# Kernel tuning notes

Hardware: AMD Instinct MI355X
Metric: run time of the kernel (lower is better)

## Reference

```python
import jax, jax.numpy as jnp
import numpy as np

R, N, B = 3, 8192, 4096
IN_DIM, HID, OUT = 256, 128, 64
EPS = 1e-5


def _bn(x, g, b):
    # BatchNorm1d in training mode: biased batch stats over dim 0
    m = jnp.mean(x, axis=0)
    v = jnp.var(x, axis=0)
    return (x - m) * jax.lax.rsqrt(v + EPS) * g + b


def setup_inputs() -> dict:
    key = jax.random.key(0)
    k1, k2, k3, k4, k5 = jax.random.split(key, 5)
    features = jax.random.normal(k1, (N, IN_DIM), dtype=jnp.float32)
    u = jax.random.uniform(k2, (R, N, N), dtype=jnp.float32)
    adj = (u < 0.01).astype(jnp.float32)
    batch_nodes = jax.random.randint(k3, (B,), 0, N, dtype=jnp.int32)
    w1 = jax.random.uniform(k4, (IN_DIM, HID), dtype=jnp.float32)  # torch.rand init
    w2 = jax.random.uniform(k5, (HID, OUT), dtype=jnp.float32)
    return {
        "features": features, "adj": adj, "batch_nodes": batch_nodes,
        "w1": w1, "w2": w2,
        "gamma1": jnp.ones((IN_DIM,), jnp.float32), "beta1": jnp.zeros((IN_DIM,), jnp.float32),
        "gamma2": jnp.ones((OUT,), jnp.float32), "beta2": jnp.zeros((OUT,), jnp.float32),
    }


def reference(features, adj, batch_nodes, w1, w2, gamma1, beta1, gamma2, beta2):
    # gather batch subgraph
    x = features[batch_nodes]                       # [B, IN_DIM]
    bA = jnp.take(jnp.take(adj, batch_nodes, axis=1), batch_nodes, axis=2)  # [R, B, B]
    xn = _bn(x, gamma1, beta1)                      # shared across relations

    def per_relation(badj):
        A = badj + jnp.eye(B, dtype=badj.dtype)
        # D_mx.inverse().sqrt() of a diagonal degree matrix == diag(deg^-1/2)
        dinv = jax.lax.rsqrt(jnp.sum(A, axis=1))    # [B]
        A_hat = A * dinv[:, None] * dinv[None, :]   # D^-1/2 A D^-1/2
        h1 = jax.nn.sigmoid(jax.nn.elu((A_hat @ xn) @ w1))   # conv1 + sigmoid
        h2 = jax.nn.elu((A_hat @ h1) @ w2)                   # conv2
        return _bn(h2, gamma2, beta2)

    embed = jax.vmap(per_relation)(bA)              # [R, B, OUT]
    return jax.nn.relu(jnp.mean(embed, axis=0))     # [B, OUT]
```

## Files before the change

kernel.cpp:

```cpp
#include <hip/hip_runtime.h>
#include <hip/hip_bf16.h>

#define RR 3
#define NN 8192
#define BB 4096
#define IN_DIM 256
#define HID 128
#define OUT 64
#define CAPD 128
#define EPS 1e-5f
#define MWN (NN / 64)
#define MLPB 16

__global__ __launch_bounds__(256) void k1_bn1_prep_k(const float* __restrict__ feat,
                                                     const int* __restrict__ bn,
                                                     const float* __restrict__ g1,
                                                     const float* __restrict__ b1,
                                                     float* __restrict__ af,
                                                     float* __restrict__ bfv,
                                                     unsigned long long* __restrict__ memb,
                                                     unsigned short* __restrict__ rankg,
                                                     unsigned short* __restrict__ nodeof,
                                                     float* __restrict__ multf,
                                                     int* __restrict__ Ucnt,
                                                     unsigned short* __restrict__ pos2slot) {
    __shared__ int smult[NN];
    __shared__ unsigned short srank[NN];
    __shared__ unsigned long long smemb[MWN];
    __shared__ int sbase[MWN + 1];
    __shared__ float ps[4], pq[4];
    int t = threadIdx.x;
    if (blockIdx.x < IN_DIM) {
        int c = blockIdx.x;
        float s = 0.f, q = 0.f;
        for (int i = t; i < BB; i += 256) {
            float v = feat[(size_t)bn[i] * IN_DIM + c];
            s += v; q += v * v;
        }
        int lane = t & 63, wv = t >> 6;
        for (int o = 32; o; o >>= 1) { s += __shfl_down(s, o); q += __shfl_down(q, o); }
        if (lane == 0) { ps[wv] = s; pq[wv] = q; }
        __syncthreads();
        if (t == 0) {
            float S = ps[0] + ps[1] + ps[2] + ps[3];
            float Q = pq[0] + pq[1] + pq[2] + pq[3];
            float m = S / BB;
            float rs = rsqrtf(Q / BB - m * m + EPS);
            float a = rs * g1[c];
            af[c]  = a;
            bfv[c] = b1[c] - m * a;
        }
        return;
    }
    for (int u = t; u < NN; u += 256) smult[u] = 0;
    __syncthreads();
    for (int i = t; i < BB; i += 256) atomicAdd(&smult[bn[i]], 1);
    __syncthreads();
    if (t < MWN) {
        unsigned long long w = 0;
        for (int b = 0; b < 64; ++b) if (smult[t * 64 + b]) w |= (1ull << b);
        smemb[t] = w;
        memb[t] = w;
    }
    __syncthreads();
    if (t == 0) {
        int acc = 0;
        for (int m = 0; m < MWN; ++m) { sbase[m] = acc; acc += (int)__popcll(smemb[m]); }
        sbase[MWN] = acc;
        *Ucnt = acc;
    }
    __syncthreads();
    if (t < MWN) {
        unsigned long long w = smemb[t];
        int p = sbase[t];
        while (w) {
            int b = __builtin_ctzll(w); w &= w - 1;
            int u = t * 64 + b;
            srank[u] = (unsigned short)p;
            rankg[u] = (unsigned short)p;
            nodeof[p] = (unsigned short)u;
            multf[p]  = (float)smult[u];
            ++p;
        }
    }
    __syncthreads();
    for (int i = t; i < BB; i += 256) pos2slot[i] = srank[bn[i]];
}

__global__ __launch_bounds__(256) void build_k(const float* __restrict__ adj,
                                               const unsigned short* __restrict__ nodeof,
                                               const int* __restrict__ Ucnt,
                                               const unsigned long long* __restrict__ memb,
                                               const unsigned short* __restrict__ rankg,
                                               const float* __restrict__ multf,
                                               unsigned* __restrict__ cols,
                                               int* __restrict__ cnt,
                                               float* __restrict__ dinv) {
    int blk = blockIdx.x;
    int r = blk >> 12, s = blk & (BB - 1);
    if (s >= *Ucnt) return;
    int u = nodeof[s];
    __shared__ unsigned char nib[2048];
    __shared__ unsigned int rawb[256];
    __shared__ unsigned long long sel[MWN];
    __shared__ int sbase[MWN + 1];
    __shared__ float pdeg[4];
    int t = threadIdx.x;
    const float4* ar4 = (const float4*)(adj + ((size_t)r * NN + u) * NN);
    #pragma unroll
    for (int ch = 0; ch < 8; ++ch) {
        float4 v = ar4[ch * 256 + t];
        nib[ch * 256 + t] = (unsigned char)((v.x != 0.f) | ((v.y != 0.f) << 1) |
                                            ((v.z != 0.f) << 2) | ((v.w != 0.f) << 3));
    }
    __syncthreads();
    {
        unsigned long long x = *(const unsigned long long*)&nib[t * 8];
        x = (x | (x >> 4))  & 0x00FF00FF00FF00FFull;
        x = (x | (x >> 8))  & 0x0000FFFF0000FFFFull;
        x = (x | (x >> 16));
        rawb[t] = (unsigned int)x;
    }
    __syncthreads();
    if (t < MWN) {
        unsigned long long w = ((unsigned long long)rawb[2 * t + 1] << 32) | rawb[2 * t];
        sel[t] = w & memb[t];
    }
    __syncthreads();
    if (t < 64) {
        int p0 = (int)__popcll(sel[2 * t]);
        int p1 = (int)__popcll(sel[2 * t + 1]);
        int x = p0 + p1, xs = x;
        for (int o = 1; o < 64; o <<= 1) { int y = __shfl_up(xs, o); if (t >= o) xs += y; }
        sbase[2 * t]     = xs - x;
        sbase[2 * t + 1] = xs - p1;
        if (t == 63) sbase[MWN] = xs;
    }
    __syncthreads();
    float wdeg = 0.f;
    if (t < MWN) {
        unsigned long long w = sel[t];
        int p = sbase[t];
        unsigned* cb = cols + (size_t)blk * CAPD;
        while (w) {
            int b = __builtin_ctzll(w); w &= w - 1;
            int v = t * 64 + b;
            int rv = rankg[v];
            if (p < CAPD) cb[p] = ((unsigned)rv << 13) | (unsigned)v;
            wdeg += multf[rv];
            ++p;
        }
    }
    int lane = t & 63, wv = t >> 6;
    for (int o = 32; o; o >>= 1) wdeg += __shfl_down(wdeg, o);
    if (lane == 0) pdeg[wv] = wdeg;
    __syncthreads();
    if (t == 0) {
        int tot = sbase[MWN];
        cnt[blk] = tot < CAPD ? tot : CAPD;
        dinv[blk] = rsqrtf(pdeg[0] + pdeg[1] + pdeg[2] + pdeg[3] + 1.0f);
    }
}

__global__ __launch_bounds__(256) void agg1_k(const float* __restrict__ feat,
                                              const unsigned* __restrict__ cols,
                                              const int* __restrict__ cnt,
                                              const float* __restrict__ dinv,
                                              const float* __restrict__ multf,
                                              const unsigned short* __restrict__ nodeof,
                                              const int* __restrict__ Ucnt,
                                              const float* __restrict__ af,
                                              const float* __restrict__ bfv,
                                              float* __restrict__ y1) {
    int blk = blockIdx.x;
    int r = blk >> 12, s = blk & (BB - 1);
    if (s >= *Ucnt) return;
    int c = threadIdx.x;
    __shared__ unsigned short snode[CAPD];
    __shared__ float swl[CAPD];
    int n = cnt[blk];
    if (c < n) {
        unsigned e = cols[(size_t)blk * CAPD + c];
        int sl = e >> 13;
        snode[c] = (unsigned short)(e & 8191u);
        swl[c] = multf[sl] * dinv[(r << 12) + sl];
    }
    __syncthreads();
    float di = dinv[blk];
    float acc = di * feat[(size_t)nodeof[s] * IN_DIM + c];
    float sw = 0.f;
    #pragma unroll 4
    for (int k = 0; k < n; ++k) {
        float w = swl[k];
        sw += w;
        acc += w * feat[(size_t)snode[k] * IN_DIM + c];
    }
    float raw = acc * di;
    float f = di * (di + sw);
    y1[(size_t)blk * IN_DIM + c] = af[c] * raw + bfv[c] * f;
}

__global__ __launch_bounds__(256) void mlp1_k(const float* __restrict__ y1,
                                              const int* __restrict__ Ucnt,
                                              const float* __restrict__ w1,
                                              float* __restrict__ h1) {
    int blk = blockIdx.x;
    int r = blk / (BB / MLPB), base = (blk % (BB / MLPB)) * MLPB;
    int U = *Ucnt;
    if (base >= U) return;
    int t = threadIdx.x;
    __shared__ float ys[MLPB][IN_DIM];
    #pragma unroll
    for (int s = 0; s < MLPB; ++s) {
        int slot = base + s;
        ys[s][t] = (slot < U) ? y1[((size_t)(r << 12) + slot) * IN_DIM + t] : 0.f;
    }
    __syncthreads();
    int c = t & 127, g = t >> 7;
    float acc[8] = {0.f};
    for (int k = 0; k < IN_DIM; ++k) {
        float wv = w1[k * HID + c];
        #pragma unroll
        for (int j = 0; j < 8; ++j) acc[j] += ys[g * 8 + j][k] * wv;
    }
    #pragma unroll
    for (int j = 0; j < 8; ++j) {
        int slot = base + g * 8 + j;
        if (slot < U) {
            float z = acc[j];
            float e = z > 0.f ? z : expm1f(z);
            h1[((size_t)(r << 12) + slot) * HID + c] = 1.f / (1.f + expf(-e));
        }
    }
}

__global__ __launch_bounds__(128) void agg2_k(const float* __restrict__ h1,
                                              const unsigned* __restrict__ cols,
                                              const int* __restrict__ cnt,
                                              const float* __restrict__ dinv,
                                              const float* __restrict__ multf,
                                              const int* __restrict__ Ucnt,
                                              float* __restrict__ y2) {
    int blk = blockIdx.x;
    int r = blk >> 12, s = blk & (BB - 1);
    if (s >= *Ucnt) return;
    int c = threadIdx.x;
    __shared__ unsigned short scl[CAPD];
    __shared__ float swl[CAPD];
    int n = cnt[blk];
    if (c < n) {
        unsigned e = cols[(size_t)blk * CAPD + c];
        int sl = e >> 13;
        scl[c] = (unsigned short)sl;
        swl[c] = multf[sl] * dinv[(r << 12) + sl];
    }
    __syncthreads();
    const float* h1r = h1 + ((size_t)(r << 12)) * HID;
    float di = dinv[blk];
    float acc = di * h1r[(size_t)s * HID + c];
    #pragma unroll 4
    for (int k = 0; k < n; ++k) {
        acc += swl[k] * h1r[(size_t)scl[k] * HID + c];
    }
    y2[(size_t)blk * HID + c] = acc * di;
}

__global__ __launch_bounds__(256) void mlp2_k(const float* __restrict__ y2,
                                              const int* __restrict__ Ucnt,
                                              const float* __restrict__ w2,
                                              float* __restrict__ h2) {
    int blk = blockIdx.x;
    int r = blk / (BB / MLPB), base = (blk % (BB / MLPB)) * MLPB;
    int U = *Ucnt;
    if (base >= U) return;
    int t = threadIdx.x;
    __shared__ float ys[MLPB][HID];
    #pragma unroll
    for (int s = t >> 7; s < MLPB; s += 2) {
        int slot = base + s;
        ys[s][t & 127] = (slot < U) ? y2[((size_t)(r << 12) + slot) * HID + (t & 127)] : 0.f;
    }
    __syncthreads();
    int c = t & 63, g = t >> 6;
    float acc[4] = {0.f};
    for (int k = 0; k < HID; ++k) {
        float wv = w2[k * OUT + c];
        #pragma unroll
        for (int j = 0; j < 4; ++j) acc[j] += ys[g * 4 + j][k] * wv;
    }
    #pragma unroll
    for (int j = 0; j < 4; ++j) {
        int slot = base + g * 4 + j;
        if (slot < U) {
            float z = acc[j];
            h2[((size_t)(r << 12) + slot) * OUT + c] = z > 0.f ? z : expm1f(z);
        }
    }
}

__global__ __launch_bounds__(256) void bn2_stats_k(const float* __restrict__ h2,
                                                   const float* __restrict__ multf,
                                                   const int* __restrict__ Ucnt,
                                                   float* __restrict__ m2,
                                                   float* __restrict__ rs2) {
    int ro = blockIdx.x;
    int r = ro >> 6, o = ro & (OUT - 1);
    int U = *Ucnt;
    float s = 0.f, q = 0.f;
    for (int sl = threadIdx.x; sl < U; sl += 256) {
        float m = multf[sl];
        float v = h2[(size_t)((r << 12) + sl) * OUT + o];
        s += m * v; q += m * v * v;
    }
    int lane = threadIdx.x & 63, wv = threadIdx.x >> 6;
    for (int off = 32; off; off >>= 1) { s += __shfl_down(s, off); q += __shfl_down(q, off); }
    __shared__ float ps[4], pq[4];
    if (lane == 0) { ps[wv] = s; pq[wv] = q; }
    __syncthreads();
    if (threadIdx.x == 0) {
        float S = ps[0] + ps[1] + ps[2] + ps[3];
        float Q = pq[0] + pq[1] + pq[2] + pq[3];
        float m = S / BB;
        float v = Q / BB - m * m;
        m2[ro] = m;
        rs2[ro] = rsqrtf(v + EPS);
    }
}

__global__ __launch_bounds__(256) void finalize_k(const float* __restrict__ h2,
                                                  const unsigned short* __restrict__ pos2slot,
                                                  const float* __restrict__ m2,
                                                  const float* __restrict__ rs2,
                                                  const float* __restrict__ g2,
                                                  const float* __restrict__ b2,
                                                  float* __restrict__ out) {
    int idx = blockIdx.x * 256 + threadIdx.x;
    if (idx >= BB * OUT) return;
    int i = idx >> 6, o = idx & (OUT - 1);
    int sl = pos2slot[i];
    float s = 0.f;
    for (int r = 0; r < RR; ++r) {
        float v = h2[(size_t)((r << 12) + sl) * OUT + o];
        s += (v - m2[r * OUT + o]) * rs2[r * OUT + o] * g2[o] + b2[o];
    }
    s *= (1.0f / RR);
    out[idx] = s > 0.f ? s : 0.f;
}

extern "C" void kernel_launch(void* const* d_in, const int* in_sizes, int n_in,
                              void* d_out, int out_size, void* d_ws, size_t ws_size,
                              hipStream_t stream) {
    const float* feat = (const float*)d_in[0];
    const float* adj  = (const float*)d_in[1];
    const int*   bn   = (const int*)d_in[2];
    const float* w1   = (const float*)d_in[3];
    const float* w2   = (const float*)d_in[4];
    const float* g1   = (const float*)d_in[5];
    const float* b1   = (const float*)d_in[6];
    const float* g2   = (const float*)d_in[7];
    const float* b2   = (const float*)d_in[8];
    float* out = (float*)d_out;

    char* ws = (char*)d_ws;
    size_t off = 0;
    auto alloc = [&](size_t bytes) { size_t o = off; off += (bytes + 255) & ~(size_t)255; return o; };
    unsigned long long* memb = (unsigned long long*)(ws + alloc(MWN * 8));
    unsigned short* rankg    = (unsigned short*)(ws + alloc(NN * 2));
    unsigned short* nodeof   = (unsigned short*)(ws + alloc(BB * 2));
    float* multf             = (float*)(ws + alloc(BB * 4));
    int* Ucnt                = (int*)(ws + alloc(4));
    unsigned short* pos2slot = (unsigned short*)(ws + alloc(BB * 2));
    float* af                = (float*)(ws + alloc(IN_DIM * 4));
    float* bfv               = (float*)(ws + alloc(IN_DIM * 4));
    float* m2                = (float*)(ws + alloc(RR * OUT * 4));
    float* rs2               = (float*)(ws + alloc(RR * OUT * 4));
    unsigned* cols           = (unsigned*)(ws + alloc((size_t)RR * BB * CAPD * 4));
    int* cnt                 = (int*)(ws + alloc((size_t)RR * BB * 4));
    float* dinv              = (float*)(ws + alloc((size_t)RR * BB * 4));
    float* y1                = (float*)(ws + alloc((size_t)RR * BB * IN_DIM * 4));
    float* h1                = (float*)(ws + alloc((size_t)RR * BB * HID * 4));
    float* y2                = (float*)(ws + alloc((size_t)RR * BB * HID * 4));
    float* h2                = (float*)(ws + alloc((size_t)RR * BB * OUT * 4));

    k1_bn1_prep_k<<<IN_DIM + 1, 256, 0, stream>>>(feat, bn, g1, b1, af, bfv,
                                                  memb, rankg, nodeof, multf, Ucnt, pos2slot);
    build_k<<<RR * BB, 256, 0, stream>>>(adj, nodeof, Ucnt, memb, rankg, multf, cols, cnt, dinv);
    agg1_k<<<RR * BB, 256, 0, stream>>>(feat, cols, cnt, dinv, multf, nodeof, Ucnt, af, bfv, y1);
    mlp1_k<<<RR * (BB / MLPB), 256, 0, stream>>>(y1, Ucnt, w1, h1);
    agg2_k<<<RR * BB, 128, 0, stream>>>(h1, cols, cnt, dinv, multf, Ucnt, y2);
    mlp2_k<<<RR * (BB / MLPB), 256, 0, stream>>>(y2, Ucnt, w2, h2);
    bn2_stats_k<<<RR * OUT, 256, 0, stream>>>(h2, multf, Ucnt, m2, rs2);
    finalize_k<<<(BB * OUT + 255) / 256, 256, 0, stream>>>(h2, pos2slot, m2, rs2, g2, b2, out);
}
```

Before: 164.9 us.

## Fuse sparse aggregation with dense MLP layers, one wave per row

Merges each aggregation kernel with the following small matmul+activation kernel, so each block of 16 rows aggregates neighbors into shared memory and then applies the weight matrix. This drops the y1/y2 intermediate buffers and two kernel launches. Each wave now handles four rows using float4 or float2 vector loads, where before each row got its own block. The trade-off is 12k blocks becoming 768 blocks, which means less parallelism for the latency-bound gathers and more shared memory per block.

```diff
diff --git a/kernel.cpp b/kernel.cpp
--- a/kernel.cpp
+++ b/kernel.cpp
@@ -10,7 +10,6 @@
 #define CAPD 128
 #define EPS 1e-5f
 #define MWN (NN / 64)
-#define MLPB 16
 
 __global__ __launch_bounds__(256) void k1_bn1_prep_k(const float* __restrict__ feat,
                                                      const int* __restrict__ bn,
@@ -162,66 +161,78 @@
     }
 }
 
-__global__ __launch_bounds__(256) void agg1_k(const float* __restrict__ feat,
-                                              const unsigned* __restrict__ cols,
-                                              const int* __restrict__ cnt,
-                                              const float* __restrict__ dinv,
-                                              const float* __restrict__ multf,
-                                              const unsigned short* __restrict__ nodeof,
-                                              const int* __restrict__ Ucnt,
-                                              const float* __restrict__ af,
-                                              const float* __restrict__ bfv,
-                                              float* __restrict__ y1) {
+__global__ __launch_bounds__(256) void aggmlp1_k(const float* __restrict__ feat,
+                                                 const unsigned* __restrict__ cols,
+                                                 const int* __restrict__ cnt,
+                                                 const float* __restrict__ dinv,
+                                                 const float* __restrict__ multf,
+                                                 const unsigned short* __restrict__ nodeof,
+                                                 const int* __restrict__ Ucnt,
+                                                 const float* __restrict__ af,
+                                                 const float* __restrict__ bfv,
+                                                 const float* __restrict__ w1,
+                                                 float* __restrict__ h1) {
     int blk = blockIdx.x;
-    int r = blk >> 12, s = blk & (BB - 1);
-    if (s >= *Ucnt) return;
-    int c = threadIdx.x;
-    __shared__ unsigned short snode[CAPD];
-    __shared__ float swl[CAPD];
-    int n = cnt[blk];
-    if (c < n) {
-        unsigned e = cols[(size_t)blk * CAPD + c];
-        int sl = e >> 13;
-        snode[c] = (unsigned short)(e & 8191u);
-        swl[c] = multf[sl] * dinv[(r << 12) + sl];
-    }
-    __syncthreads();
-    float di = dinv[blk];
-    float acc = di * feat[(size_t)nodeof[s] * IN_DIM + c];
-    float sw = 0.f;
-    #pragma unroll 4
-    for (int k = 0; k < n; ++k) {
-        float w = swl[k];
-        sw += w;
-        acc += w * feat[(size_t)snode[k] * IN_DIM + c];
-    }
-    float raw = acc * di;
-    float f = di * (di + sw);
-    y1[(size_t)blk * IN_DIM + c] = af[c] * raw + bfv[c] * f;
-}
-
-__global__ __launch_bounds__(256) void mlp1_k(const float* __restrict__ y1,
-                                              const int* __restrict__ Ucnt,
-                                              const float* __restrict__ w1,
-                                              float* __restrict__ h1) {
-    int blk = blockIdx.x;
-    int r = blk / (BB / MLPB), base = (blk % (BB / MLPB)) * MLPB;
+    int r = blk >> 8, base = (blk & 255) << 4;
     int U = *Ucnt;
     if (base >= U) return;
-    int t = threadIdx.x;
-    __shared__ float ys[MLPB][IN_DIM];
-    #pragma unroll
-    for (int s = 0; s < MLPB; ++s) {
-        int slot = base + s;
-        ys[s][t] = (slot < U) ? y1[((size_t)(r << 12) + slot) * IN_DIM + t] : 0.f;
+    int t = threadIdx.x, lane = t & 63, wv = t >> 6;
+    __shared__ unsigned short snode[16][CAPD];
+    __shared__ float swl[16][CAPD];
+    __shared__ float ys[16][IN_DIM];
+    __shared__ float sdii[16], ssw[16];
+    __shared__ int sn[16];
+    for (int s16 = wv; s16 < 16; s16 += 4) {
+        int slot = base + s16;
+        int n = (slot < U) ? cnt[(r << 12) + slot] : 0;
+        if (lane == 0) { sn[s16] = n; sdii[s16] = (slot < U) ? dinv[(r << 12) + slot] : 0.f; }
+        size_t cb = ((size_t)(r << 12) + slot) * CAPD;
+        float swsum = 0.f;
+        for (int idx = lane; idx < n; idx += 64) {
+            unsigned e = cols[cb + idx];
+            int sl = e >> 13;
+            snode[s16][idx] = (unsigned short)(e & 8191u);
+            float w = multf[sl] * dinv[(r << 12) + sl];
+            swl[s16][idx] = w;
+            swsum += w;
+        }
+        for (int o = 32; o; o >>= 1) swsum += __shfl_down(swsum, o);
+        if (lane == 0) ssw[s16] = swsum;
+    }
+    __syncthreads();
+    int c4 = lane << 2;
+    for (int j = 0; j < 4; ++j) {
+        int s16 = (wv << 2) + j;
+        int slot = base + s16;
+        if (slot >= U) { *(float4*)&ys[s16][c4] = make_float4(0.f, 0.f, 0.f, 0.f); continue; }
+        int n = sn[s16];
+        float di = sdii[s16];
+        float4 v = ((const float4*)(feat + (size_t)nodeof[slot] * IN_DIM))[lane];
+        float4 acc;
+        acc.x = di * v.x; acc.y = di * v.y; acc.z = di * v.z; acc.w = di * v.w;
+        #pragma unroll 4
+        for (int k = 0; k < n; ++k) {
+            float w = swl[s16][k];
+            float4 x = ((const float4*)(feat + (size_t)snode[s16][k] * IN_DIM))[lane];
+            acc.x += w * x.x; acc.y += w * x.y; acc.z += w * x.z; acc.w += w * x.w;
+        }
+        float f = di * (di + ssw[s16]);
+        float4 a4 = *(const float4*)(af + c4);
+        float4 b4 = *(const float4*)(bfv + c4);
+        float4 o;
+        o.x = a4.x * (acc.x * di) + b4.x * f;
+        o.y = a4.y * (acc.y * di) + b4.y * f;
+        o.z = a4.z * (acc.z * di) + b4.z * f;
+        o.w = a4.w * (acc.w * di) + b4.w * f;
+        *(float4*)&ys[s16][c4] = o;
     }
     __syncthreads();
     int c = t & 127, g = t >> 7;
     float acc[8] = {0.f};
     for (int k = 0; k < IN_DIM; ++k) {
-        float wv = w1[k * HID + c];
+        float wvl = w1[k * HID + c];
         #pragma unroll
-        for (int j = 0; j < 8; ++j) acc[j] += ys[g * 8 + j][k] * wv;
+        for (int j = 0; j < 8; ++j) acc[j] += ys[g * 8 + j][k] * wvl;
     }
     #pragma unroll
     for (int j = 0; j < 8; ++j) {
@@ -234,59 +245,63 @@
     }
 }
 
-__global__ __launch_bounds__(128) void agg2_k(const float* __restrict__ h1,
-                                              const unsigned* __restrict__ cols,
-                                              const int* __restrict__ cnt,
-                                              const float* __restrict__ dinv,
-                                              const float* __restrict__ multf,
-                                              const int* __restrict__ Ucnt,
-                                              float* __restrict__ y2) {
+__global__ __launch_bounds__(256) void aggmlp2_k(const float* __restrict__ h1,
+                                                 const unsigned* __restrict__ cols,
+                                                 const int* __restrict__ cnt,
+                                                 const float* __restrict__ dinv,
+                                                 const float* __restrict__ multf,
+                                                 const int* __restrict__ Ucnt,
+                                                 const float* __restrict__ w2,
+                                                 float* __restrict__ h2) {
     int blk = blockIdx.x;
-    int r = blk >> 12, s = blk & (BB - 1);
-    if (s >= *Ucnt) return;
-    int c = threadIdx.x;
-    __shared__ unsigned short scl[CAPD];
-    __shared__ float swl[CAPD];
-    int n = cnt[blk];
-    if (c < n) {
-        unsigned e = cols[(size_t)blk * CAPD + c];
-        int sl = e >> 13;
-        scl[c] = (unsigned short)sl;
-        swl[c] = multf[sl] * dinv[(r << 12) + sl];
-    }
-    __syncthreads();
-    const float* h1r = h1 + ((size_t)(r << 12)) * HID;
-    float di = dinv[blk];
-    float acc = di * h1r[(size_t)s * HID + c];
-    #pragma unroll 4
-    for (int k = 0; k < n; ++k) {
-        acc += swl[k] * h1r[(size_t)scl[k] * HID + c];
-    }
-    y2[(size_t)blk * HID + c] = acc * di;
-}
-
-__global__ __launch_bounds__(256) void mlp2_k(const float* __restrict__ y2,
-                                              const int* __restrict__ Ucnt,
-                                              const float* __restrict__ w2,
-                                              float* __restrict__ h2) {
-    int blk = blockIdx.x;
-    int r = blk / (BB / MLPB), base = (blk % (BB / MLPB)) * MLPB;
+    int r = blk >> 8, base = (blk & 255) << 4;
     int U = *Ucnt;
     if (base >= U) return;
-    int t = threadIdx.x;
-    __shared__ float ys[MLPB][HID];
-    #pragma unroll
-    for (int s = t >> 7; s < MLPB; s += 2) {
-        int slot = base + s;
-        ys[s][t & 127] = (slot < U) ? y2[((size_t)(r << 12) + slot) * HID + (t & 127)] : 0.f;
+    int t = threadIdx.x, lane = t & 63, wv = t >> 6;
+    __shared__ unsigned short scl[16][CAPD];
+    __shared__ float swl[16][CAPD];
+    __shared__ float ys[16][HID];
+    __shared__ float sdii[16];
+    __shared__ int sn[16];
+    for (int s16 = wv; s16 < 16; s16 += 4) {
+        int slot = base + s16;
+        int n = (slot < U) ? cnt[(r << 12) + slot] : 0;
+        if (lane == 0) { sn[s16] = n; sdii[s16] = (slot < U) ? dinv[(r << 12) + slot] : 0.f; }
+        size_t cb = ((size_t)(r << 12) + slot) * CAPD;
+        for (int idx = lane; idx < n; idx += 64) {
+            unsigned e = cols[cb + idx];
+            int sl = e >> 13;
+            scl[s16][idx] = (unsigned short)sl;
+            swl[s16][idx] = multf[sl] * dinv[(r << 12) + sl];
+        }
+    }
+    __syncthreads();
+    const float* h1r = h1 + ((size_t)(r << 12)) * HID;
+    int c2 = lane << 1;
+    for (int j = 0; j < 4; ++j) {
+        int s16 = (wv << 2) + j;
+        int slot = base + s16;
+        if (slot >= U) { ys[s16][c2] = 0.f; ys[s16][c2 + 1] = 0.f; continue; }
+        int n = sn[s16];
+        float di = sdii[s16];
+        float2 v = ((const float2*)(h1r + (size_t)slot * HID))[lane];
+        float ax = di * v.x, ay = di * v.y;
+        #pragma unroll 4
+        for (int k = 0; k < n; ++k) {
+            float w = swl[s16][k];
+            float2 x = ((const float2*)(h1r + (size_t)scl[s16][k] * HID))[lane];
+            ax += w * x.x; ay += w * x.y;
+        }
+        ys[s16][c2] = ax * di;
+        ys[s16][c2 + 1] = ay * di;
     }
     __syncthreads();
     int c = t & 63, g = t >> 6;
     float acc[4] = {0.f};
     for (int k = 0; k < HID; ++k) {
-        float wv = w2[k * OUT + c];
+        float wvl = w2[k * OUT + c];
         #pragma unroll
-        for (int j = 0; j < 4; ++j) acc[j] += ys[g * 4 + j][k] * wv;
+        for (int j = 0; j < 4; ++j) acc[j] += ys[g * 4 + j][k] * wvl;
     }
     #pragma unroll
     for (int j = 0; j < 4; ++j) {
@@ -377,18 +392,15 @@
     unsigned* cols           = (unsigned*)(ws + alloc((size_t)RR * BB * CAPD * 4));
     int* cnt                 = (int*)(ws + alloc((size_t)RR * BB * 4));
     float* dinv              = (float*)(ws + alloc((size_t)RR * BB * 4));
-    float* y1                = (float*)(ws + alloc((size_t)RR * BB * IN_DIM * 4));
     float* h1                = (float*)(ws + alloc((size_t)RR * BB * HID * 4));
-    float* y2                = (float*)(ws + alloc((size_t)RR * BB * HID * 4));
     float* h2                = (float*)(ws + alloc((size_t)RR * BB * OUT * 4));
 
     k1_bn1_prep_k<<<IN_DIM + 1, 256, 0, stream>>>(feat, bn, g1, b1, af, bfv,
                                                   memb, rankg, nodeof, multf, Ucnt, pos2slot);
     build_k<<<RR * BB, 256, 0, stream>>>(adj, nodeof, Ucnt, memb, rankg, multf, cols, cnt, dinv);
-    agg1_k<<<RR * BB, 256, 0, stream>>>(feat, cols, cnt, dinv, multf, nodeof, Ucnt, af, bfv, y1);
-    mlp1_k<<<RR * (BB / MLPB), 256, 0, stream>>>(y1, Ucnt, w1, h1);
-    agg2_k<<<RR * BB, 128, 0, stream>>>(h1, cols, cnt, dinv, multf, Ucnt, y2);
-    mlp2_k<<<RR * (BB / MLPB), 256, 0, stream>>>(y2, Ucnt, w2, h2);
+    aggmlp1_k<<<RR * (BB / 16), 256, 0, stream>>>(feat, cols, cnt, dinv, multf, nodeof, Ucnt,
+                                                  af, bfv, w1, h1);
+    aggmlp2_k<<<RR * (BB / 16), 256, 0, stream>>>(h1, cols, cnt, dinv, multf, Ucnt, w2, h2);
     bn2_stats_k<<<RR * OUT, 256, 0, stream>>>(h2, multf, Ucnt, m2, rs2);
     finalize_k<<<(BB * OUT + 255) / 256, 256, 0, stream>>>(h2, pos2slot, m2, rs2, g2, b2, out);
 }
```

After: 154.1 us, median of 3. 1.07x faster.
